# Kernel tuning notes

Hardware: AMD Instinct MI355X
Metric: run time of the kernel (lower is better)

Reference implementation:

```python
import jax, jax.numpy as jnp
import numpy as np

H = 128
N_GENE = 100000
N_VAR = 200000
E = 500000


def setup_inputs() -> dict:
    key = jax.random.key(0)
    ks = jax.random.split(key, 24)
    s = 0.05
    inp = {
        "emb_gene": jax.random.normal(ks[0], (N_GENE, H), jnp.float32) * s,
        "emb_var": jax.random.normal(ks[1], (N_VAR, H), jnp.float32) * s,
        "Wl1_gv": jax.random.normal(ks[2], (H, H), jnp.float32) * s,
        "bl1_gv": jnp.zeros((H,), jnp.float32),
        "Wr1_gv": jax.random.normal(ks[3], (H, H), jnp.float32) * s,
        "Wl1_vg": jax.random.normal(ks[4], (H, H), jnp.float32) * s,
        "bl1_vg": jnp.zeros((H,), jnp.float32),
        "Wr1_vg": jax.random.normal(ks[5], (H, H), jnp.float32) * s,
        "Wl2_gv": jax.random.normal(ks[6], (H, H), jnp.float32) * s,
        "bl2_gv": jnp.zeros((H,), jnp.float32),
        "Wr2_gv": jax.random.normal(ks[7], (H, H), jnp.float32) * s,
        "Wl2_vg": jax.random.normal(ks[8], (H, H), jnp.float32) * s,
        "bl2_vg": jnp.zeros((H,), jnp.float32),
        "Wr2_vg": jax.random.normal(ks[9], (H, H), jnp.float32) * s,
        "A1": jax.random.normal(ks[10], (H, H), jnp.float32) * s,
        "b1": jnp.zeros((H,), jnp.float32),
        "A2": jax.random.normal(ks[11], (8, H), jnp.float32) * s,
        "b2": jnp.zeros((8,), jnp.float32),
        "src_gv": jax.random.randint(ks[12], (E,), 0, N_GENE, jnp.int32),
        "dst_gv": jax.random.randint(ks[13], (E,), 0, N_VAR, jnp.int32),
        "src_vg": jax.random.randint(ks[14], (E,), 0, N_VAR, jnp.int32),
        "dst_vg": jax.random.randint(ks[15], (E,), 0, N_GENE, jnp.int32),
    }
    return inp


def _sage(x_src, x_dst, src, dst, Wl, bl, Wr):
    # PyG SAGEConv: lin_l(mean_{j->i} x_src[j]) + lin_r(x_dst[i])
    msg = x_src[src]                                             # [E, H] gather
    agg = jax.ops.segment_sum(msg, dst, num_segments=x_dst.shape[0])
    cnt = jax.ops.segment_sum(jnp.ones_like(src, x_src.dtype), dst,
                              num_segments=x_dst.shape[0])
    mean = agg / jnp.maximum(cnt, 1.0)[:, None]
    return mean @ Wl.T + bl + x_dst @ Wr.T


def reference(emb_gene, emb_var,
              Wl1_gv, bl1_gv, Wr1_gv, Wl1_vg, bl1_vg, Wr1_vg,
              Wl2_gv, bl2_gv, Wr2_gv, Wl2_vg, bl2_vg, Wr2_vg,
              A1, b1, A2, b2,
              src_gv, dst_gv, src_vg, dst_vg):
    # layer 1: gene->variant updates variant; variant->gene updates gene
    h_var = _sage(emb_gene, emb_var, src_gv, dst_gv, Wl1_gv, bl1_gv, Wr1_gv)
    h_gene = _sage(emb_var, emb_gene, src_vg, dst_vg, Wl1_vg, bl1_vg, Wr1_vg)
    z_gene = jax.nn.relu(h_gene)
    z_var = jax.nn.relu(h_var)
    # layer 2
    z_var2 = _sage(z_gene, z_var, src_gv, dst_gv, Wl2_gv, bl2_gv, Wr2_gv)
    z_gene2 = _sage(z_var, z_gene, src_vg, dst_vg, Wl2_vg, bl2_vg, Wr2_vg)
    # adversarial head on 'gene' (GradReverse is identity in forward)
    hdn = jax.nn.relu(z_gene2 @ A1.T + b1)
    adv_gene = hdn @ A2.T + b2
    return (z_gene2, z_var2, adv_gene)
```

## Files before the change

### kernel.cpp

```cpp
#include <hip/hip_runtime.h>
#include <hip/hip_bf16.h>

typedef unsigned short u16;
typedef unsigned int u32;
typedef __attribute__((ext_vector_type(8))) short bf16x8;
typedef __attribute__((ext_vector_type(4))) float f32x4;

#define NG 100000
#define NV 200000
#define NE 500000
#define HD 128
#define NALL (NG + NV)
#define EALL (2 * NE)

__device__ __forceinline__ float bflo(u32 w) { return __uint_as_float(w << 16); }
__device__ __forceinline__ float bfhi(u32 w) { return __uint_as_float(w & 0xffff0000u); }
__device__ __forceinline__ u16 f2bf(float f) {
    __hip_bfloat16 h = __float2bfloat16(f);
    u16 u; __builtin_memcpy(&u, &h, 2); return u;
}
__device__ __forceinline__ u32 pk2(float a, float b) {
    return (u32)f2bf(a) | ((u32)f2bf(b) << 16);
}

__global__ __launch_bounds__(256) void cvt_kernel(const float* __restrict__ g,
                                                  const float* __restrict__ v,
                                                  u16* __restrict__ out) {
    size_t slot = (size_t)blockIdx.x * 256 + threadIdx.x;
    size_t off = slot * 8;
    if (off >= (size_t)NALL * HD) return;
    const float* p = (off < (size_t)NG * HD) ? (g + off) : (v + (off - (size_t)NG * HD));
    float4 a = *(const float4*)p;
    float4 b = *(const float4*)(p + 4);
    uint4 pk;
    pk.x = pk2(a.x, a.y); pk.y = pk2(a.z, a.w);
    pk.z = pk2(b.x, b.y); pk.w = pk2(b.z, b.w);
    *(uint4*)(out + off) = pk;
}

__global__ __launch_bounds__(256) void wcvt_kernel(
    const float* w0, const float* w1, const float* w2, const float* w3,
    const float* w4, const float* w5, const float* w6, const float* w7,
    const float* w8, u16* __restrict__ out)
{
    const float* Ws[9] = {w0, w1, w2, w3, w4, w5, w6, w7, w8};
    const float* W = Ws[blockIdx.x];
    u16* o = out + (size_t)blockIdx.x * 16384;
    int tid = threadIdx.x;
#pragma unroll
    for (int it = 0; it < 8; ++it) {
        int slot = it * 256 + tid;
        int f = slot >> 6, l = slot & 63;
        int kt = f >> 3, ct = f & 7;
        int row = ct * 16 + (l & 15);
        int kof = kt * 32 + (l >> 4) * 8;
        const float* wp = W + (size_t)row * HD + kof;
        float4 x = *(const float4*)wp;
        float4 y = *(const float4*)(wp + 4);
        uint4 pk;
        pk.x = pk2(x.x, x.y); pk.y = pk2(x.z, x.w);
        pk.z = pk2(y.x, y.y); pk.w = pk2(y.z, y.w);
        *(uint4*)(o + (size_t)slot * 8) = pk;
    }
}

__global__ __launch_bounds__(256) void hist2_kernel(const int* __restrict__ dst_gv,
                                                    const int* __restrict__ dst_vg,
                                                    int* __restrict__ deg) {
    int t = blockIdx.x * 256 + threadIdx.x;
    if (t < NE)            atomicAdd(&deg[dst_gv[t]], 1);
    else if (t < EALL)     atomicAdd(&deg[NV + dst_vg[t - NE]], 1);
}

__global__ __launch_bounds__(256) void scan1_kernel(const int* __restrict__ deg,
                                                    int* __restrict__ excl,
                                                    int* __restrict__ bsum, int N) {
    __shared__ int lds[256];
    int tid = threadIdx.x;
    int base = blockIdx.x * 2048 + tid * 8;
    int v[8]; int s = 0;
#pragma unroll
    for (int i = 0; i < 8; ++i) { v[i] = (base + i < N) ? deg[base + i] : 0; s += v[i]; }
    lds[tid] = s;
    __syncthreads();
    for (int off = 1; off < 256; off <<= 1) {
        int x = (tid >= off) ? lds[tid - off] : 0;
        __syncthreads();
        lds[tid] += x;
        __syncthreads();
    }
    int run = lds[tid] - s;
#pragma unroll
    for (int i = 0; i < 8; ++i) {
        if (base + i < N) excl[base + i] = run;
        run += v[i];
    }
    if (tid == 255) bsum[blockIdx.x] = lds[255];
}

__global__ void scan2_kernel(int* __restrict__ bsum, int nb) {
    if (threadIdx.x == 0 && blockIdx.x == 0) {
        int run = 0;
        for (int i = 0; i < nb; ++i) { int t = bsum[i]; bsum[i] = run; run += t; }
    }
}

__global__ __launch_bounds__(256) void scan3_kernel(int* __restrict__ rs,
                                                    int* __restrict__ cur,
                                                    const int* __restrict__ bsum, int N) {
    int i = blockIdx.x * 256 + threadIdx.x;
    if (i < N) {
        int v = rs[i] + bsum[i >> 11];
        rs[i] = v;
        cur[i] = v;
    }
    if (i == 0) rs[N] = EALL;
}

__global__ __launch_bounds__(256) void escatter2_kernel(const int* __restrict__ src_gv,
                                                        const int* __restrict__ dst_gv,
                                                        const int* __restrict__ src_vg,
                                                        const int* __restrict__ dst_vg,
                                                        int* __restrict__ cur,
                                                        int* __restrict__ esrc) {
    int t = blockIdx.x * 256 + threadIdx.x;
    if (t < NE) {
        int p = atomicAdd(&cur[dst_gv[t]], 1);
        esrc[p] = src_gv[t];
    } else if (t < EALL) {
        int e = t - NE;
        int p = atomicAdd(&cur[NV + dst_vg[e]], 1);
        esrc[p] = NG + src_vg[e];
    }
}

__global__ __launch_bounds__(256) void aggregate_kernel(const u16* __restrict__ X,
                                                        const int* __restrict__ rs,
                                                        const int* __restrict__ esrc,
                                                        u16* __restrict__ aggb) {
    u32 t = blockIdx.x * 256 + threadIdx.x;
    int row = t >> 4, c = t & 15;
    if (row >= NALL) return;
    int e0 = rs[row], e1 = rs[row + 1];
    float s[8] = {0.f, 0.f, 0.f, 0.f, 0.f, 0.f, 0.f, 0.f};
    for (int e = e0; e < e1; ++e) {
        const u16* p = X + (size_t)esrc[e] * HD + c * 8;
        uint4 u = *(const uint4*)p;
        u32 w[4] = {u.x, u.y, u.z, u.w};
#pragma unroll
        for (int i = 0; i < 4; ++i) { s[2 * i] += bflo(w[i]); s[2 * i + 1] += bfhi(w[i]); }
    }
    float rcv = 1.f / fmaxf((float)(e1 - e0), 1.f);
    uint4 pk;
    pk.x = pk2(s[0] * rcv, s[1] * rcv);
    pk.y = pk2(s[2] * rcv, s[3] * rcv);
    pk.z = pk2(s[4] * rcv, s[5] * rcv);
    pk.w = pk2(s[6] * rcv, s[7] * rcv);
    *(uint4*)(aggb + (size_t)row * HD + c * 8) = pk;
}

template <int RELU, int OBF16>
__global__ __launch_bounds__(256, 4) void sage_mfma2_kernel(
    const u16* __restrict__ aggb,
    const u16* __restrict__ Xb,
    const u16* __restrict__ wf_v,
    const u16* __restrict__ wf_g,
    const float* __restrict__ b_v, const float* __restrict__ b_g,
    float* __restrict__ outf_v, float* __restrict__ outf_g,
    u16* __restrict__ outb_v, u16* __restrict__ outb_g,
    int nvb)
{
    __shared__ __align__(16) float lds_t[4][16][132];
    const bool isVar = (int)blockIdx.x < nvb;
    const int bseg = isVar ? blockIdx.x : blockIdx.x - nvb;
    const int Nseg = isVar ? NV : NG;
    const u16* Aseg = aggb + (size_t)(isVar ? 0 : NV) * HD;
    const u16* Xseg = Xb + (size_t)(isVar ? NG : 0) * HD;
    const u16* wf = isVar ? wf_v : wf_g;
    const float* bias = isVar ? b_v : b_g;
    float* outf = isVar ? outf_v : outf_g;
    u16* outb = isVar ? outb_v : outb_g;

    const int tid = threadIdx.x;
    const int lane = tid & 63;
    const int wid = tid >> 6;
    const int m0 = bseg * 128 + wid * 32;
    const int lr = lane & 15, lg = lane >> 4;

    f32x4 acc[2][8];
#pragma unroll
    for (int rt = 0; rt < 2; ++rt)
#pragma unroll
        for (int ct = 0; ct < 8; ++ct) acc[rt][ct] = (f32x4){0.f, 0.f, 0.f, 0.f};

#pragma unroll
    for (int ph = 0; ph < 2; ++ph) {
        const u16* A = (ph == 0) ? Aseg : Xseg;
        const u16* wp = wf + ph * 16384;
        bf16x8 a[4][2];
#pragma unroll
        for (int kt = 0; kt < 4; ++kt)
#pragma unroll
            for (int rt = 0; rt < 2; ++rt) {
                int row = m0 + rt * 16 + lr; if (row > Nseg - 1) row = Nseg - 1;
                a[kt][rt] = *(const bf16x8*)(A + (size_t)row * HD + kt * 32 + lg * 8);
            }
#pragma unroll
        for (int kt = 0; kt < 4; ++kt)
#pragma unroll
            for (int ct = 0; ct < 8; ++ct) {
                bf16x8 w = *(const bf16x8*)(wp + (size_t)(((kt * 8 + ct) << 6) + lane) * 8);
#pragma unroll
                for (int rt = 0; rt < 2; ++rt)
                    acc[rt][ct] = __builtin_amdgcn_mfma_f32_16x16x32_bf16(
                        a[kt][rt], w, acc[rt][ct], 0, 0, 0);
            }
    }

    float bv[8];
#pragma unroll
    for (int ct = 0; ct < 8; ++ct) bv[ct] = bias[ct * 16 + lr];

#pragma unroll
    for (int rt = 0; rt < 2; ++rt) {
#pragma unroll
        for (int ct = 0; ct < 8; ++ct)
#pragma unroll
            for (int r = 0; r < 4; ++r) {
                float v = acc[rt][ct][r] + bv[ct];
                if (RELU) v = fmaxf(v, 0.f);
                lds_t[wid][lg * 4 + r][ct * 16 + lr] = v;
            }
        __syncthreads();
        if (OBF16 == 0) {
#pragma unroll
            for (int i = 0; i < 8; ++i) {
                int row16 = i * 2 + (lane >> 5);
                int colb = (lane & 31) * 4;
                f32x4 v = *(const f32x4*)&lds_t[wid][row16][colb];
                int grow = m0 + rt * 16 + row16;
                if (grow < Nseg) *(f32x4*)(outf + (size_t)grow * HD + colb) = v;
            }
        } else {
#pragma unroll
            for (int i = 0; i < 4; ++i) {
                int row16 = i * 4 + (lane >> 4);
                int colb = (lane & 15) * 8;
                f32x4 v0 = *(const f32x4*)&lds_t[wid][row16][colb];
                f32x4 v1 = *(const f32x4*)&lds_t[wid][row16][colb + 4];
                uint4 pk;
                pk.x = pk2(v0[0], v0[1]); pk.y = pk2(v0[2], v0[3]);
                pk.z = pk2(v1[0], v1[1]); pk.w = pk2(v1[2], v1[3]);
                int grow = m0 + rt * 16 + row16;
                if (grow < Nseg) *(uint4*)(outb + (size_t)grow * HD + colb) = pk;
            }
        }
        __syncthreads();
    }
}

__global__ __launch_bounds__(256, 4) void head_kernel(
    const float* __restrict__ g2,
    const u16* __restrict__ wfA1,
    const float* __restrict__ b1,
    const float* __restrict__ A2,
    const float* __restrict__ b2,
    float* __restrict__ adv)
{
    __shared__ __align__(16) u16 lds_h[4][16][136];
    const int tid = threadIdx.x;
    const int lane = tid & 63;
    const int wid = tid >> 6;
    const int m0 = blockIdx.x * 128 + wid * 32;
    const int lr = lane & 15, lg = lane >> 4;

    bf16x8 a2f[4];
#pragma unroll
    for (int kt = 0; kt < 4; ++kt) {
        union { u16 s[8]; bf16x8 v; } u;
        if (lr < 8) {
            const float* p = A2 + (size_t)lr * HD + kt * 32 + lg * 8;
            float4 x = *(const float4*)p;
            float4 y = *(const float4*)(p + 4);
            u.s[0] = f2bf(x.x); u.s[1] = f2bf(x.y); u.s[2] = f2bf(x.z); u.s[3] = f2bf(x.w);
            u.s[4] = f2bf(y.x); u.s[5] = f2bf(y.y); u.s[6] = f2bf(y.z); u.s[7] = f2bf(y.w);
        } else {
#pragma unroll
            for (int i = 0; i < 8; ++i) u.s[i] = 0;
        }
        a2f[kt] = u.v;
    }

    f32x4 acc[2][8];
#pragma unroll
    for (int rt = 0; rt < 2; ++rt)
#pragma unroll
        for (int ct = 0; ct < 8; ++ct) acc[rt][ct] = (f32x4){0.f, 0.f, 0.f, 0.f};

#pragma unroll
    for (int kt = 0; kt < 4; ++kt) {
        bf16x8 a[2];
#pragma unroll
        for (int rt = 0; rt < 2; ++rt) {
            int row = m0 + rt * 16 + lr; if (row > NG - 1) row = NG - 1;
            const float* p = g2 + (size_t)row * HD + kt * 32 + lg * 8;
            float4 x = *(const float4*)p;
            float4 y = *(const float4*)(p + 4);
            union { u16 s[8]; bf16x8 v; } u;
            u.s[0] = f2bf(x.x); u.s[1] = f2bf(x.y); u.s[2] = f2bf(x.z); u.s[3] = f2bf(x.w);
            u.s[4] = f2bf(y.x); u.s[5] = f2bf(y.y); u.s[6] = f2bf(y.z); u.s[7] = f2bf(y.w);
            a[rt] = u.v;
        }
#pragma unroll
        for (int ct = 0; ct < 8; ++ct) {
            bf16x8 w = *(const bf16x8*)(wfA1 + (size_t)(((kt * 8 + ct) << 6) + lane) * 8);
#pragma unroll
            for (int rt = 0; rt < 2; ++rt)
                acc[rt][ct] = __builtin_amdgcn_mfma_f32_16x16x32_bf16(
                    a[rt], w, acc[rt][ct], 0, 0, 0);
        }
    }

    float b1v[8];
#pragma unroll
    for (int ct = 0; ct < 8; ++ct) b1v[ct] = b1[ct * 16 + lr];
    float b2v = (lr < 8) ? b2[lr] : 0.f;

#pragma unroll
    for (int rt = 0; rt < 2; ++rt) {
#pragma unroll
        for (int ct = 0; ct < 8; ++ct)
#pragma unroll
            for (int r = 0; r < 4; ++r) {
                float v = fmaxf(acc[rt][ct][r] + b1v[ct], 0.f);
                lds_h[wid][lg * 4 + r][ct * 16 + lr] = f2bf(v);
            }
        __syncthreads();
        f32x4 av = (f32x4){0.f, 0.f, 0.f, 0.f};
#pragma unroll
        for (int kt = 0; kt < 4; ++kt) {
            bf16x8 h = *(const bf16x8*)&lds_h[wid][lr][kt * 32 + lg * 8];
            av = __builtin_amdgcn_mfma_f32_16x16x32_bf16(h, a2f[kt], av, 0, 0, 0);
        }
        if (lr < 8) {
#pragma unroll
            for (int r = 0; r < 4; ++r) {
                int grow = m0 + rt * 16 + lg * 4 + r;
                if (grow < NG) adv[(size_t)grow * 8 + lr] = av[r] + b2v;
            }
        }
        __syncthreads();
    }
}

extern "C" void kernel_launch(void* const* d_in, const int* in_sizes, int n_in,
                              void* d_out, int out_size, void* d_ws, size_t ws_size,
                              hipStream_t stream)
{
    const float* emb_gene = (const float*)d_in[0];
    const float* emb_var  = (const float*)d_in[1];
    const float* Wl1_gv = (const float*)d_in[2];
    const float* bl1_gv = (const float*)d_in[3];
    const float* Wr1_gv = (const float*)d_in[4];
    const float* Wl1_vg = (const float*)d_in[5];
    const float* bl1_vg = (const float*)d_in[6];
    const float* Wr1_vg = (const float*)d_in[7];
    const float* Wl2_gv = (const float*)d_in[8];
    const float* bl2_gv = (const float*)d_in[9];
    const float* Wr2_gv = (const float*)d_in[10];
    const float* Wl2_vg = (const float*)d_in[11];
    const float* bl2_vg = (const float*)d_in[12];
    const float* Wr2_vg = (const float*)d_in[13];
    const float* A1 = (const float*)d_in[14];
    const float* b1 = (const float*)d_in[15];
    const float* A2 = (const float*)d_in[16];
    const float* b2 = (const float*)d_in[17];
    const int* src_gv = (const int*)d_in[18];
    const int* dst_gv = (const int*)d_in[19];
    const int* src_vg = (const int*)d_in[20];
    const int* dst_vg = (const int*)d_in[21];

    char* ws = (char*)d_ws;
    u16* embb  = (u16*)(ws);
    u16* zb    = (u16*)(ws + 76800000);
    u16* aggb  = (u16*)(ws + 153600000);
    u16* wfrag = (u16*)(ws + 230400000);
    int* rs    = (int*)(ws + 230700000);
    int* esrc  = (int*)(ws + 232000000);
    int* deg   = (int*)(ws + 236000000);
    int* cur   = (int*)(ws + 237200000);
    int* bsum  = (int*)(ws + 238400000);

    float* out       = (float*)d_out;
    float* out_gene2 = out;
    float* out_var2  = out + (size_t)NG * HD;
    float* out_adv   = out + (size_t)(NG + NV) * HD;

    const int NB = (NALL + 2047) / 2048;
    const int EB2 = (EALL + 255) / 256;
    const int NVB = (NV + 127) / 128;
    const int NGB = (NG + 127) / 128;
    const int CVB = (int)(((size_t)NALL * HD / 8 + 255) / 256);

    hipMemsetAsync(deg, 0, (size_t)NALL * 4, stream);
    cvt_kernel<<<CVB, 256, 0, stream>>>(emb_gene, emb_var, embb);
    wcvt_kernel<<<9, 256, 0, stream>>>(Wl1_gv, Wr1_gv, Wl1_vg, Wr1_vg,
                                       Wl2_gv, Wr2_gv, Wl2_vg, Wr2_vg, A1, wfrag);
    hist2_kernel<<<EB2, 256, 0, stream>>>(dst_gv, dst_vg, deg);
    scan1_kernel<<<NB, 256, 0, stream>>>(deg, rs, bsum, NALL);
    scan2_kernel<<<1, 64, 0, stream>>>(bsum, NB);
    scan3_kernel<<<(NALL + 255) / 256, 256, 0, stream>>>(rs, cur, bsum, NALL);
    escatter2_kernel<<<EB2, 256, 0, stream>>>(src_gv, dst_gv, src_vg, dst_vg, cur, esrc);

    aggregate_kernel<<<NALL * 16 / 256, 256, 0, stream>>>(embb, rs, esrc, aggb);
    sage_mfma2_kernel<1, 1><<<NVB + NGB, 256, 0, stream>>>(aggb, embb,
        wfrag + 0 * 16384, wfrag + 2 * 16384, bl1_gv, bl1_vg,
        nullptr, nullptr,
        zb + (size_t)NG * HD, zb,
        NVB);

    aggregate_kernel<<<NALL * 16 / 256, 256, 0, stream>>>(zb, rs, esrc, aggb);
    sage_mfma2_kernel<0, 0><<<NVB + NGB, 256, 0, stream>>>(aggb, zb,
        wfrag + 4 * 16384, wfrag + 6 * 16384, bl2_gv, bl2_vg,
        out_var2, out_gene2,
        nullptr, nullptr,
        NVB);

    head_kernel<<<NGB, 256, 0, stream>>>(out_gene2, wfrag + 8 * 16384, b1, A2, b2, out_adv);
}
```

Before: 491.7 us.

## Fuse neighbor mean aggregation into SAGE MFMA kernel via swizzled LDS tile

Each SAGE block now gathers and averages its 128 destination rows' neighbor features directly into a swizzled bf16 LDS tile, then feeds the MFMA from LDS. The separate aggregate kernel and its aggb round trip through global memory are removed. The gather loop is also unrolled by two to keep more loads in flight. The tradeoff is that gather latency now sits inside the MFMA kernel, which has a fixed 4-blocks-per-CU occupancy and an extra barrier.

```diff
diff --git a/kernel.cpp b/kernel.cpp
--- a/kernel.cpp
+++ b/kernel.cpp
@@ -134,47 +134,24 @@
     }
 }
 
-__global__ __launch_bounds__(256) void aggregate_kernel(const u16* __restrict__ X,
-                                                        const int* __restrict__ rs,
-                                                        const int* __restrict__ esrc,
-                                                        u16* __restrict__ aggb) {
-    u32 t = blockIdx.x * 256 + threadIdx.x;
-    int row = t >> 4, c = t & 15;
-    if (row >= NALL) return;
-    int e0 = rs[row], e1 = rs[row + 1];
-    float s[8] = {0.f, 0.f, 0.f, 0.f, 0.f, 0.f, 0.f, 0.f};
-    for (int e = e0; e < e1; ++e) {
-        const u16* p = X + (size_t)esrc[e] * HD + c * 8;
-        uint4 u = *(const uint4*)p;
-        u32 w[4] = {u.x, u.y, u.z, u.w};
-#pragma unroll
-        for (int i = 0; i < 4; ++i) { s[2 * i] += bflo(w[i]); s[2 * i + 1] += bfhi(w[i]); }
-    }
-    float rcv = 1.f / fmaxf((float)(e1 - e0), 1.f);
-    uint4 pk;
-    pk.x = pk2(s[0] * rcv, s[1] * rcv);
-    pk.y = pk2(s[2] * rcv, s[3] * rcv);
-    pk.z = pk2(s[4] * rcv, s[5] * rcv);
-    pk.w = pk2(s[6] * rcv, s[7] * rcv);
-    *(uint4*)(aggb + (size_t)row * HD + c * 8) = pk;
-}
-
 template <int RELU, int OBF16>
-__global__ __launch_bounds__(256, 4) void sage_mfma2_kernel(
-    const u16* __restrict__ aggb,
+__global__ __launch_bounds__(256, 4) void fused_sage_kernel(
     const u16* __restrict__ Xb,
-    const u16* __restrict__ wf_v,
-    const u16* __restrict__ wf_g,
+    const int* __restrict__ rs,
+    const int* __restrict__ esrc,
+    const u16* __restrict__ wf_v, const u16* __restrict__ wf_g,
     const float* __restrict__ b_v, const float* __restrict__ b_g,
     float* __restrict__ outf_v, float* __restrict__ outf_g,
     u16* __restrict__ outb_v, u16* __restrict__ outb_g,
     int nvb)
 {
-    __shared__ __align__(16) float lds_t[4][16][132];
+    __shared__ __align__(16) char ldsbuf[33792];
+    u16* atile = (u16*)ldsbuf;
+
     const bool isVar = (int)blockIdx.x < nvb;
     const int bseg = isVar ? blockIdx.x : blockIdx.x - nvb;
     const int Nseg = isVar ? NV : NG;
-    const u16* Aseg = aggb + (size_t)(isVar ? 0 : NV) * HD;
+    const int gseg = isVar ? 0 : NV;
     const u16* Xseg = Xb + (size_t)(isVar ? NG : 0) * HD;
     const u16* wf = isVar ? wf_v : wf_g;
     const float* bias = isVar ? b_v : b_g;
@@ -187,23 +164,64 @@
     const int m0 = bseg * 128 + wid * 32;
     const int lr = lane & 15, lg = lane >> 4;
 
+    {
+        const int c = tid & 15;
+        for (int it = 0; it < 8; ++it) {
+            int lrow = it * 16 + (tid >> 4);
+            int srow = bseg * 128 + lrow;
+            float s[8] = {0.f, 0.f, 0.f, 0.f, 0.f, 0.f, 0.f, 0.f};
+            float rcv = 0.f;
+            if (srow < Nseg) {
+                int e0 = rs[gseg + srow], e1 = rs[gseg + srow + 1];
+                int e = e0;
+                for (; e + 2 <= e1; e += 2) {
+                    const u16* p0 = Xb + (size_t)esrc[e] * HD + c * 8;
+                    const u16* p1 = Xb + (size_t)esrc[e + 1] * HD + c * 8;
+                    uint4 u0 = *(const uint4*)p0;
+                    uint4 u1 = *(const uint4*)p1;
+                    u32 w0[4] = {u0.x, u0.y, u0.z, u0.w};
+                    u32 w1[4] = {u1.x, u1.y, u1.z, u1.w};
+#pragma unroll
+                    for (int i = 0; i < 4; ++i) {
+                        s[2 * i] += bflo(w0[i]) + bflo(w1[i]);
+                        s[2 * i + 1] += bfhi(w0[i]) + bfhi(w1[i]);
+                    }
+                }
+                if (e < e1) {
+                    const u16* p = Xb + (size_t)esrc[e] * HD + c * 8;
+                    uint4 u = *(const uint4*)p;
+                    u32 w[4] = {u.x, u.y, u.z, u.w};
+#pragma unroll
+                    for (int i = 0; i < 4; ++i) { s[2 * i] += bflo(w[i]); s[2 * i + 1] += bfhi(w[i]); }
+                }
+                rcv = 1.f / fmaxf((float)(e1 - e0), 1.f);
+            }
+            uint4 pk;
+            pk.x = pk2(s[0] * rcv, s[1] * rcv);
+            pk.y = pk2(s[2] * rcv, s[3] * rcv);
+            pk.z = pk2(s[4] * rcv, s[5] * rcv);
+            pk.w = pk2(s[6] * rcv, s[7] * rcv);
+            *(uint4*)(atile + lrow * 128 + ((c ^ (lrow & 15)) << 3)) = pk;
+        }
+    }
+    __syncthreads();
+
     f32x4 acc[2][8];
 #pragma unroll
     for (int rt = 0; rt < 2; ++rt)
 #pragma unroll
         for (int ct = 0; ct < 8; ++ct) acc[rt][ct] = (f32x4){0.f, 0.f, 0.f, 0.f};
 
-#pragma unroll
-    for (int ph = 0; ph < 2; ++ph) {
-        const u16* A = (ph == 0) ? Aseg : Xseg;
-        const u16* wp = wf + ph * 16384;
+    {
+        const u16* wp = wf;
         bf16x8 a[4][2];
 #pragma unroll
         for (int kt = 0; kt < 4; ++kt)
 #pragma unroll
             for (int rt = 0; rt < 2; ++rt) {
-                int row = m0 + rt * 16 + lr; if (row > Nseg - 1) row = Nseg - 1;
-                a[kt][rt] = *(const bf16x8*)(A + (size_t)row * HD + kt * 32 + lg * 8);
+                int lrow = wid * 32 + rt * 16 + lr;
+                int ck = (kt * 4 + lg) ^ (lrow & 15);
+                a[kt][rt] = *(const bf16x8*)(atile + lrow * 128 + (ck << 3));
             }
 #pragma unroll
         for (int kt = 0; kt < 4; ++kt)
@@ -216,11 +234,34 @@
                         a[kt][rt], w, acc[rt][ct], 0, 0, 0);
             }
     }
+    {
+        const u16* wp = wf + 16384;
+        bf16x8 a[4][2];
+#pragma unroll
+        for (int kt = 0; kt < 4; ++kt)
+#pragma unroll
+            for (int rt = 0; rt < 2; ++rt) {
+                int row = m0 + rt * 16 + lr; if (row > Nseg - 1) row = Nseg - 1;
+                a[kt][rt] = *(const bf16x8*)(Xseg + (size_t)row * HD + kt * 32 + lg * 8);
+            }
+#pragma unroll
+        for (int kt = 0; kt < 4; ++kt)
+#pragma unroll
+            for (int ct = 0; ct < 8; ++ct) {
+                bf16x8 w = *(const bf16x8*)(wp + (size_t)(((kt * 8 + ct) << 6) + lane) * 8);
+#pragma unroll
+                for (int rt = 0; rt < 2; ++rt)
+                    acc[rt][ct] = __builtin_amdgcn_mfma_f32_16x16x32_bf16(
+                        a[kt][rt], w, acc[rt][ct], 0, 0, 0);
+            }
+    }
 
     float bv[8];
 #pragma unroll
     for (int ct = 0; ct < 8; ++ct) bv[ct] = bias[ct * 16 + lr];
 
+    __syncthreads();
+    float (*lds_t)[16][132] = (float (*)[16][132])ldsbuf;
 #pragma unroll
     for (int rt = 0; rt < 2; ++rt) {
 #pragma unroll
@@ -383,13 +424,12 @@
     char* ws = (char*)d_ws;
     u16* embb  = (u16*)(ws);
     u16* zb    = (u16*)(ws + 76800000);
-    u16* aggb  = (u16*)(ws + 153600000);
-    u16* wfrag = (u16*)(ws + 230400000);
-    int* rs    = (int*)(ws + 230700000);
-    int* esrc  = (int*)(ws + 232000000);
-    int* deg   = (int*)(ws + 236000000);
-    int* cur   = (int*)(ws + 237200000);
-    int* bsum  = (int*)(ws + 238400000);
+    u16* wfrag = (u16*)(ws + 153600000);
+    int* rs    = (int*)(ws + 154000000);
+    int* esrc  = (int*)(ws + 155300000);
+    int* deg   = (int*)(ws + 159300000);
+    int* cur   = (int*)(ws + 160500000);
+    int* bsum  = (int*)(ws + 161700000);
 
     float* out       = (float*)d_out;
     float* out_gene2 = out;
@@ -412,15 +452,13 @@
     scan3_kernel<<<(NALL + 255) / 256, 256, 0, stream>>>(rs, cur, bsum, NALL);
     escatter2_kernel<<<EB2, 256, 0, stream>>>(src_gv, dst_gv, src_vg, dst_vg, cur, esrc);
 
-    aggregate_kernel<<<NALL * 16 / 256, 256, 0, stream>>>(embb, rs, esrc, aggb);
-    sage_mfma2_kernel<1, 1><<<NVB + NGB, 256, 0, stream>>>(aggb, embb,
+    fused_sage_kernel<1, 1><<<NVB + NGB, 256, 0, stream>>>(embb, rs, esrc,
         wfrag + 0 * 16384, wfrag + 2 * 16384, bl1_gv, bl1_vg,
         nullptr, nullptr,
         zb + (size_t)NG * HD, zb,
         NVB);
 
-    aggregate_kernel<<<NALL * 16 / 256, 256, 0, stream>>>(zb, rs, esrc, aggb);
-    sage_mfma2_kernel<0, 0><<<NVB + NGB, 256, 0, stream>>>(aggb, zb,
+    fused_sage_kernel<0, 0><<<NVB + NGB, 256, 0, stream>>>(zb, rs, esrc,
         wfrag + 4 * 16384, wfrag + 6 * 16384, bl2_gv, bl2_vg,
         out_var2, out_gene2,
         nullptr, nullptr,
```

After: 477.3 us. -2.9%, faster.
